# Performance work log

Measured on AMD Instinct MI355X. Metric: run time of the kernel, lower is better.

The kernel has to match this reference:

```python
import jax, jax.numpy as jnp
import numpy as np

B, T, D = 4096, 200, 64
H = 32  # hidden units of score MLP
NEG_INF = jnp.float32(-2**32 + 1)


def setup_inputs() -> dict:
    key = jax.random.key(0)
    k1, k2, k3, k4, k5 = jax.random.split(key, 5)
    query = jax.random.normal(k1, (B, 1, D), dtype=jnp.float32)
    keys = jax.random.normal(k2, (B, T, D), dtype=jnp.float32)
    mask = jax.random.randint(k3, (B, T), 0, 2) > 0
    mask = mask.at[:, 0].set(True)  # ensure at least one valid key per row
    # Glorot-normal-ish init for the tiny score MLP
    W1 = jax.random.normal(k4, (3 * D, H), dtype=jnp.float32) * jnp.sqrt(2.0 / (3 * D + H))
    b1 = jnp.zeros((H,), dtype=jnp.float32)
    W2 = jax.random.normal(k5, (H, 1), dtype=jnp.float32) * jnp.sqrt(2.0 / (H + 1))
    b2 = jnp.zeros((1,), dtype=jnp.float32)
    return {"query": query, "keys": keys, "mask": mask,
            "W1": W1, "b1": b1, "W2": W2, "b2": b2}


def reference(query, keys, mask, W1, b1, W2, b2):
    b, t, d = keys.shape
    q = jnp.broadcast_to(query, (b, t, d))            # tile query over seq
    att_in = jnp.concatenate([q, keys, q - keys], axis=-1)   # [B,T,3D]
    h = jax.nn.sigmoid(att_in @ W1 + b1)              # [B,T,H]
    score = (h @ W2 + b2)[..., 0]                     # [B,T]
    score = jnp.where(mask, score, NEG_INF)
    w = jax.nn.softmax(score, axis=-1)                # [B,T]
    out = jnp.einsum('bt,btd->bd', w, keys)           # weighted key sum
    return out[:, None, :]                            # [B,1,D]
```

## Files before the change

kernel.cpp:

```cpp
#include <hip/hip_runtime.h>
#include <hip/hip_bf16.h>


#define B 4096
#define T 200
#define D 64
#define H 32
#define LOG2E 1.44269504088896340736f
#define SOFF 16.0f

typedef __attribute__((ext_vector_type(8))) short short8;
typedef __attribute__((ext_vector_type(4))) float f32x4;


__global__ __launch_bounds__(256) void prep_kernel(
        const float* __restrict__ W1,
        const float* __restrict__ b1,
        const float* __restrict__ query,
        float*       __restrict__ qa_ws,
        unsigned short* __restrict__ wkf)
{
    int blk = blockIdx.x;
    int n = blk * 256 + threadIdx.x;
    if (blk < (B * H) / 256) {
        int b = n >> 5;
        int j = n & 31;
        const float* qb = query + (size_t)b * D;
        float acc = b1[j];
        #pragma unroll 8
        for (int i = 0; i < D; ++i)
            acc = fmaf(qb[i], W1[i * H + j] + W1[(128 + i) * H + j], acc);
        qa_ws[n] = acc;
    } else {
        int m = n - (B * H);
        int e  = m & 7;
        int l  = (m >> 3) & 63;
        int fs = m >> 9;
        int ntile = fs >> 1, kstep = fs & 1;
        int k = kstep * 32 + (l >> 4) * 8 + e;
        int j = ntile * 16 + (l & 15);
        float v = W1[(64 + k) * H + j] - W1[(128 + k) * H + j];
        __hip_bfloat16 hv = __float2bfloat16(v);
        wkf[m] = __builtin_bit_cast(unsigned short, hv);
    }
}

__device__ __forceinline__ unsigned short bf16u(float x) {
    __hip_bfloat16 h = __float2bfloat16(x);
    return __builtin_bit_cast(unsigned short, h);
}

__global__ __launch_bounds__(256, 5) void attn_pool_kernel(
        const float* __restrict__ keys,
        const int*   __restrict__ mask,
        const unsigned short* __restrict__ wkf,
        const float* __restrict__ qa_all,
        const float* __restrict__ W2,
        float*       __restrict__ out)
{
    __shared__ float part[4][64];
    __shared__ float denw[4];

    const int tid  = threadIdx.x;
    const int b    = blockIdx.x;
    const int wv   = tid >> 6;
    const int lane = tid & 63;
    const int quad = lane >> 4;
    const int l15  = lane & 15;

    const short8* wf = reinterpret_cast<const short8*>(wkf);
    short8 bf0 = wf[0 * 64 + lane];
    short8 bf1 = wf[1 * 64 + lane];
    short8 bf2 = wf[2 * 64 + lane];
    short8 bf3 = wf[3 * 64 + lane];

    const float* qa = qa_all + (size_t)b * H;
    const float qa0 = qa[l15];
    const float qa1 = qa[16 + l15];
    const float w20 = W2[l15];
    const float w21 = W2[16 + l15];

    const float4* krow = reinterpret_cast<const float4*>(keys + (size_t)b * (T * D));
    const int*    mrow = mask + (size_t)b * T;

    float acc[16];
    #pragma unroll
    for (int e = 0; e < 16; ++e) acc[e] = 0.0f;
    float den = 0.0f;

    for (int m0 = wv; m0 < 13; m0 += 4) {
        const int t  = m0 * 16 + l15;
        const int tr = (t < T) ? t : (T - 1);

        float4 k0 = krow[tr * 16 + quad * 2 + 0];
        float4 k1 = krow[tr * 16 + quad * 2 + 1];
        float4 k2 = krow[tr * 16 + 8 + quad * 2 + 0];
        float4 k3 = krow[tr * 16 + 8 + quad * 2 + 1];
        int mval = mrow[tr];

        short8 a0, a1;
        a0[0] = (short)bf16u(k0.x); a0[1] = (short)bf16u(k0.y);
        a0[2] = (short)bf16u(k0.z); a0[3] = (short)bf16u(k0.w);
        a0[4] = (short)bf16u(k1.x); a0[5] = (short)bf16u(k1.y);
        a0[6] = (short)bf16u(k1.z); a0[7] = (short)bf16u(k1.w);
        a1[0] = (short)bf16u(k2.x); a1[1] = (short)bf16u(k2.y);
        a1[2] = (short)bf16u(k2.z); a1[3] = (short)bf16u(k2.w);
        a1[4] = (short)bf16u(k3.x); a1[5] = (short)bf16u(k3.y);
        a1[6] = (short)bf16u(k3.z); a1[7] = (short)bf16u(k3.w);

        f32x4 c0 = {0.f, 0.f, 0.f, 0.f};
        f32x4 c1 = {0.f, 0.f, 0.f, 0.f};
        c0 = __builtin_amdgcn_mfma_f32_16x16x32_bf16(a0, bf0, c0, 0, 0, 0);
        c0 = __builtin_amdgcn_mfma_f32_16x16x32_bf16(a1, bf1, c0, 0, 0, 0);
        c1 = __builtin_amdgcn_mfma_f32_16x16x32_bf16(a0, bf2, c1, 0, 0, 0);
        c1 = __builtin_amdgcn_mfma_f32_16x16x32_bf16(a1, bf3, c1, 0, 0, 0);

        float p[4];
        #pragma unroll
        for (int r = 0; r < 4; ++r) {
            float x0 = c0[r] + qa0;
            float x1 = c1[r] + qa1;
            float s0 = __builtin_amdgcn_rcpf(1.0f + exp2f(-x0 * LOG2E));
            float s1 = __builtin_amdgcn_rcpf(1.0f + exp2f(-x1 * LOG2E));
            p[r] = fmaf(s0, w20, s1 * w21);
        }
        #pragma unroll
        for (int r = 0; r < 4; ++r) {
            #pragma unroll
            for (int off = 1; off <= 8; off <<= 1)
                p[r] += __shfl_xor(p[r], off, 64);
        }
        const int addr = (l15 >> 2) << 6;
        int q0 = __builtin_amdgcn_ds_bpermute(addr, __builtin_bit_cast(int, p[0]));
        int q1 = __builtin_amdgcn_ds_bpermute(addr, __builtin_bit_cast(int, p[1]));
        int q2 = __builtin_amdgcn_ds_bpermute(addr, __builtin_bit_cast(int, p[2]));
        int q3 = __builtin_amdgcn_ds_bpermute(addr, __builtin_bit_cast(int, p[3]));
        const int rsel = l15 & 3;
        int s01 = (rsel & 1) ? q1 : q0;
        int s23 = (rsel & 1) ? q3 : q2;
        float st = __builtin_bit_cast(float, (rsel & 2) ? s23 : s01);

        float w = ((t < T) && (mval != 0)) ? exp2f((st - SOFF) * LOG2E) : 0.0f;
        den += w;

        acc[0]  = fmaf(w, k0.x, acc[0]);  acc[1]  = fmaf(w, k0.y, acc[1]);
        acc[2]  = fmaf(w, k0.z, acc[2]);  acc[3]  = fmaf(w, k0.w, acc[3]);
        acc[4]  = fmaf(w, k1.x, acc[4]);  acc[5]  = fmaf(w, k1.y, acc[5]);
        acc[6]  = fmaf(w, k1.z, acc[6]);  acc[7]  = fmaf(w, k1.w, acc[7]);
        acc[8]  = fmaf(w, k2.x, acc[8]);  acc[9]  = fmaf(w, k2.y, acc[9]);
        acc[10] = fmaf(w, k2.z, acc[10]); acc[11] = fmaf(w, k2.w, acc[11]);
        acc[12] = fmaf(w, k3.x, acc[12]); acc[13] = fmaf(w, k3.y, acc[13]);
        acc[14] = fmaf(w, k3.z, acc[14]); acc[15] = fmaf(w, k3.w, acc[15]);
    }

    #pragma unroll
    for (int off = 1; off <= 8; off <<= 1) {
        #pragma unroll
        for (int e = 0; e < 16; ++e)
            acc[e] += __shfl_xor(acc[e], off, 64);
        den += __shfl_xor(den, off, 64);
    }

    if (l15 == 0) {
        #pragma unroll
        for (int e = 0; e < 8; ++e) {
            part[wv][quad * 8 + e]      = acc[e];
            part[wv][32 + quad * 8 + e] = acc[8 + e];
        }
        if (quad == 0) denw[wv] = den;
    }
    __syncthreads();

    if (tid < 64) {
        float dtot = (denw[0] + denw[1]) + (denw[2] + denw[3]);
        float v = (part[0][tid] + part[1][tid]) + (part[2][tid] + part[3][tid]);
        out[(size_t)b * D + tid] = v * __builtin_amdgcn_rcpf(dtot);
    }
}

extern "C" void kernel_launch(void* const* d_in, const int* in_sizes, int n_in,
                              void* d_out, int out_size, void* d_ws, size_t ws_size,
                              hipStream_t stream) {
    const float* query = (const float*)d_in[0];
    const float* keys  = (const float*)d_in[1];
    const int*   mask  = (const int*)d_in[2];
    const float* W1    = (const float*)d_in[3];
    const float* b1    = (const float*)d_in[4];
    const float* W2    = (const float*)d_in[5];

    float* qa = (float*)d_ws;
    unsigned short* wkf = (unsigned short*)(qa + B * H);

    prep_kernel<<<(B * H) / 256 + 8, 256, 0, stream>>>(W1, b1, query, qa, wkf);
    attn_pool_kernel<<<B, 256, 0, stream>>>(keys, mask, wkf, qa, W2, (float*)d_out);
}
```

Before: 305.1 us.

## Split each batch row into per-wave tiles with atomic accumulation and a finalize pass

Instead of one block per batch row where four waves loop over 13 tiles unevenly, each wave now handles exactly one 16-key tile of one row. Partial numerators are reduced in shared memory and added with global float atomics, and a new finalize kernel divides by the accumulated denominator. The prep kernel also zeroes the accumulation buffers. This is meant to fix load imbalance (13 tiles across 4 waves) and raise parallelism, at the cost of one extra kernel launch, atomic traffic, and nondeterministic summation order.

```diff
diff --git a/kernel.cpp b/kernel.cpp
--- a/kernel.cpp
+++ b/kernel.cpp
@@ -8,6 +8,8 @@
 #define H 32
 #define LOG2E 1.44269504088896340736f
 #define SOFF 16.0f
+#define NTILE 13
+#define PITCH 68
 
 typedef __attribute__((ext_vector_type(8))) short short8;
 typedef __attribute__((ext_vector_type(4))) float f32x4;
@@ -17,12 +19,12 @@
         const float* __restrict__ W1,
         const float* __restrict__ b1,
         const float* __restrict__ query,
-        float*       __restrict__ qa_ws,
-        unsigned short* __restrict__ wkf)
+        float*       __restrict__ ws)
 {
     int blk = blockIdx.x;
-    int n = blk * 256 + threadIdx.x;
-    if (blk < (B * H) / 256) {
+    int tid = threadIdx.x;
+    if (blk < 512) {
+        int n = blk * 256 + tid;
         int b = n >> 5;
         int j = n & 31;
         const float* qb = query + (size_t)b * D;
@@ -30,9 +32,9 @@
         #pragma unroll 8
         for (int i = 0; i < D; ++i)
             acc = fmaf(qb[i], W1[i * H + j] + W1[(128 + i) * H + j], acc);
-        qa_ws[n] = acc;
-    } else {
-        int m = n - (B * H);
+        ws[n] = acc;
+    } else if (blk < 520) {
+        int m = (blk - 512) * 256 + tid;
         int e  = m & 7;
         int l  = (m >> 3) & 63;
         int fs = m >> 9;
@@ -41,7 +43,12 @@
         int j = ntile * 16 + (l & 15);
         float v = W1[(64 + k) * H + j] - W1[(128 + k) * H + j];
         __hip_bfloat16 hv = __float2bfloat16(v);
-        wkf[m] = __builtin_bit_cast(unsigned short, hv);
+        reinterpret_cast<unsigned short*>(ws + 131072)[m] =
+            __builtin_bit_cast(unsigned short, hv);
+    } else {
+        int z = (blk - 520) * 256 + tid;
+        float4 zz = {0.f, 0.f, 0.f, 0.f};
+        reinterpret_cast<float4*>(ws + 132096)[z] = zz;
     }
 }
 
@@ -50,23 +57,26 @@
     return __builtin_bit_cast(unsigned short, h);
 }
 
-__global__ __launch_bounds__(256, 5) void attn_pool_kernel(
+__global__ __launch_bounds__(256) void attn_pool_kernel(
         const float* __restrict__ keys,
         const int*   __restrict__ mask,
         const unsigned short* __restrict__ wkf,
         const float* __restrict__ qa_all,
         const float* __restrict__ W2,
-        float*       __restrict__ out)
+        float*       __restrict__ num,
+        float*       __restrict__ den)
 {
-    __shared__ float part[4][64];
-    __shared__ float denw[4];
+    __shared__ float wkbuf[4][16 * PITCH];
 
     const int tid  = threadIdx.x;
-    const int b    = blockIdx.x;
     const int wv   = tid >> 6;
     const int lane = tid & 63;
     const int quad = lane >> 4;
     const int l15  = lane & 15;
+
+    const int gid  = blockIdx.x * 4 + wv;
+    const int b    = (int)(((unsigned)gid * 20165u) >> 18);
+    const int tile = gid - b * NTILE;
 
     const short8* wf = reinterpret_cast<const short8*>(wkf);
     short8 bf0 = wf[0 * 64 + lane];
@@ -80,102 +90,90 @@
     const float w20 = W2[l15];
     const float w21 = W2[16 + l15];
 
+    const int t  = tile * 16 + l15;
+    const int tr = (t < T) ? t : (T - 1);
+
     const float4* krow = reinterpret_cast<const float4*>(keys + (size_t)b * (T * D));
-    const int*    mrow = mask + (size_t)b * T;
+    float4 k0 = krow[tr * 16 + quad * 2 + 0];
+    float4 k1 = krow[tr * 16 + quad * 2 + 1];
+    float4 k2 = krow[tr * 16 + 8 + quad * 2 + 0];
+    float4 k3 = krow[tr * 16 + 8 + quad * 2 + 1];
+    const int mval = mask[(size_t)b * T + tr];
 
-    float acc[16];
+    short8 a0, a1;
+    a0[0] = (short)bf16u(k0.x); a0[1] = (short)bf16u(k0.y);
+    a0[2] = (short)bf16u(k0.z); a0[3] = (short)bf16u(k0.w);
+    a0[4] = (short)bf16u(k1.x); a0[5] = (short)bf16u(k1.y);
+    a0[6] = (short)bf16u(k1.z); a0[7] = (short)bf16u(k1.w);
+    a1[0] = (short)bf16u(k2.x); a1[1] = (short)bf16u(k2.y);
+    a1[2] = (short)bf16u(k2.z); a1[3] = (short)bf16u(k2.w);
+    a1[4] = (short)bf16u(k3.x); a1[5] = (short)bf16u(k3.y);
+    a1[6] = (short)bf16u(k3.z); a1[7] = (short)bf16u(k3.w);
+
+    f32x4 c0 = {0.f, 0.f, 0.f, 0.f};
+    f32x4 c1 = {0.f, 0.f, 0.f, 0.f};
+    c0 = __builtin_amdgcn_mfma_f32_16x16x32_bf16(a0, bf0, c0, 0, 0, 0);
+    c0 = __builtin_amdgcn_mfma_f32_16x16x32_bf16(a1, bf1, c0, 0, 0, 0);
+    c1 = __builtin_amdgcn_mfma_f32_16x16x32_bf16(a0, bf2, c1, 0, 0, 0);
+    c1 = __builtin_amdgcn_mfma_f32_16x16x32_bf16(a1, bf3, c1, 0, 0, 0);
+
+    float p[4];
     #pragma unroll
-    for (int e = 0; e < 16; ++e) acc[e] = 0.0f;
-    float den = 0.0f;
+    for (int r = 0; r < 4; ++r) {
+        float x0 = c0[r] + qa0;
+        float x1 = c1[r] + qa1;
+        float s0 = __builtin_amdgcn_rcpf(1.0f + exp2f(-x0 * LOG2E));
+        float s1 = __builtin_amdgcn_rcpf(1.0f + exp2f(-x1 * LOG2E));
+        p[r] = fmaf(s0, w20, s1 * w21);
+    }
+    #pragma unroll
+    for (int r = 0; r < 4; ++r) {
+        #pragma unroll
+        for (int off = 1; off <= 8; off <<= 1)
+            p[r] += __shfl_xor(p[r], off, 64);
+    }
+    const int addr = (l15 >> 2) << 6;
+    int q0 = __builtin_amdgcn_ds_bpermute(addr, __builtin_bit_cast(int, p[0]));
+    int q1 = __builtin_amdgcn_ds_bpermute(addr, __builtin_bit_cast(int, p[1]));
+    int q2 = __builtin_amdgcn_ds_bpermute(addr, __builtin_bit_cast(int, p[2]));
+    int q3 = __builtin_amdgcn_ds_bpermute(addr, __builtin_bit_cast(int, p[3]));
+    const int rsel = l15 & 3;
+    int s01 = (rsel & 1) ? q1 : q0;
+    int s23 = (rsel & 1) ? q3 : q2;
+    float st = __builtin_bit_cast(float, (rsel & 2) ? s23 : s01);
 
-    for (int m0 = wv; m0 < 13; m0 += 4) {
-        const int t  = m0 * 16 + l15;
-        const int tr = (t < T) ? t : (T - 1);
+    const float w = ((t < T) && (mval != 0)) ? exp2f((st - SOFF) * LOG2E) : 0.0f;
 
-        float4 k0 = krow[tr * 16 + quad * 2 + 0];
-        float4 k1 = krow[tr * 16 + quad * 2 + 1];
-        float4 k2 = krow[tr * 16 + 8 + quad * 2 + 0];
-        float4 k3 = krow[tr * 16 + 8 + quad * 2 + 1];
-        int mval = mrow[tr];
+    float* wb = wkbuf[wv];
+    float4 wk0 = {w * k0.x, w * k0.y, w * k0.z, w * k0.w};
+    float4 wk1 = {w * k1.x, w * k1.y, w * k1.z, w * k1.w};
+    float4 wk2 = {w * k2.x, w * k2.y, w * k2.z, w * k2.w};
+    float4 wk3 = {w * k3.x, w * k3.y, w * k3.z, w * k3.w};
+    *reinterpret_cast<float4*>(&wb[l15 * PITCH + quad * 8 + 0]) = wk0;
+    *reinterpret_cast<float4*>(&wb[l15 * PITCH + quad * 8 + 4]) = wk1;
+    *reinterpret_cast<float4*>(&wb[l15 * PITCH + 32 + quad * 8 + 0]) = wk2;
+    *reinterpret_cast<float4*>(&wb[l15 * PITCH + 32 + quad * 8 + 4]) = wk3;
 
-        short8 a0, a1;
-        a0[0] = (short)bf16u(k0.x); a0[1] = (short)bf16u(k0.y);
-        a0[2] = (short)bf16u(k0.z); a0[3] = (short)bf16u(k0.w);
-        a0[4] = (short)bf16u(k1.x); a0[5] = (short)bf16u(k1.y);
-        a0[6] = (short)bf16u(k1.z); a0[7] = (short)bf16u(k1.w);
-        a1[0] = (short)bf16u(k2.x); a1[1] = (short)bf16u(k2.y);
-        a1[2] = (short)bf16u(k2.z); a1[3] = (short)bf16u(k2.w);
-        a1[4] = (short)bf16u(k3.x); a1[5] = (short)bf16u(k3.y);
-        a1[6] = (short)bf16u(k3.z); a1[7] = (short)bf16u(k3.w);
+    float dw = w;
+    #pragma unroll
+    for (int off = 1; off <= 8; off <<= 1)
+        dw += __shfl_xor(dw, off, 64);
 
-        f32x4 c0 = {0.f, 0.f, 0.f, 0.f};
-        f32x4 c1 = {0.f, 0.f, 0.f, 0.f};
-        c0 = __builtin_amdgcn_mfma_f32_16x16x32_bf16(a0, bf0, c0, 0, 0, 0);
-        c0 = __builtin_amdgcn_mfma_f32_16x16x32_bf16(a1, bf1, c0, 0, 0, 0);
-        c1 = __builtin_amdgcn_mfma_f32_16x16x32_bf16(a0, bf2, c1, 0, 0, 0);
-        c1 = __builtin_amdgcn_mfma_f32_16x16x32_bf16(a1, bf3, c1, 0, 0, 0);
+    float colsum = 0.0f;
+    #pragma unroll
+    for (int tt = 0; tt < 16; ++tt)
+        colsum += wb[tt * PITCH + lane];
 
-        float p[4];
-        #pragma unroll
-        for (int r = 0; r < 4; ++r) {
-            float x0 = c0[r] + qa0;
-            float x1 = c1[r] + qa1;
-            float s0 = __builtin_amdgcn_rcpf(1.0f + exp2f(-x0 * LOG2E));
-            float s1 = __builtin_amdgcn_rcpf(1.0f + exp2f(-x1 * LOG2E));
-            p[r] = fmaf(s0, w20, s1 * w21);
-        }
-        #pragma unroll
-        for (int r = 0; r < 4; ++r) {
-            #pragma unroll
-            for (int off = 1; off <= 8; off <<= 1)
-                p[r] += __shfl_xor(p[r], off, 64);
-        }
-        const int addr = (l15 >> 2) << 6;
-        int q0 = __builtin_amdgcn_ds_bpermute(addr, __builtin_bit_cast(int, p[0]));
-        int q1 = __builtin_amdgcn_ds_bpermute(addr, __builtin_bit_cast(int, p[1]));
-        int q2 = __builtin_amdgcn_ds_bpermute(addr, __builtin_bit_cast(int, p[2]));
-        int q3 = __builtin_amdgcn_ds_bpermute(addr, __builtin_bit_cast(int, p[3]));
-        const int rsel = l15 & 3;
-        int s01 = (rsel & 1) ? q1 : q0;
-        int s23 = (rsel & 1) ? q3 : q2;
-        float st = __builtin_bit_cast(float, (rsel & 2) ? s23 : s01);
+    atomicAdd(&num[(size_t)b * D + lane], colsum);
+    if (lane == 0) atomicAdd(&den[b], dw);
+}
 
-        float w = ((t < T) && (mval != 0)) ? exp2f((st - SOFF) * LOG2E) : 0.0f;
-        den += w;
-
-        acc[0]  = fmaf(w, k0.x, acc[0]);  acc[1]  = fmaf(w, k0.y, acc[1]);
-        acc[2]  = fmaf(w, k0.z, acc[2]);  acc[3]  = fmaf(w, k0.w, acc[3]);
-        acc[4]  = fmaf(w, k1.x, acc[4]);  acc[5]  = fmaf(w, k1.y, acc[5]);
-        acc[6]  = fmaf(w, k1.z, acc[6]);  acc[7]  = fmaf(w, k1.w, acc[7]);
-        acc[8]  = fmaf(w, k2.x, acc[8]);  acc[9]  = fmaf(w, k2.y, acc[9]);
-        acc[10] = fmaf(w, k2.z, acc[10]); acc[11] = fmaf(w, k2.w, acc[11]);
-        acc[12] = fmaf(w, k3.x, acc[12]); acc[13] = fmaf(w, k3.y, acc[13]);
-        acc[14] = fmaf(w, k3.z, acc[14]); acc[15] = fmaf(w, k3.w, acc[15]);
-    }
-
-    #pragma unroll
-    for (int off = 1; off <= 8; off <<= 1) {
-        #pragma unroll
-        for (int e = 0; e < 16; ++e)
-            acc[e] += __shfl_xor(acc[e], off, 64);
-        den += __shfl_xor(den, off, 64);
-    }
-
-    if (l15 == 0) {
-        #pragma unroll
-        for (int e = 0; e < 8; ++e) {
-            part[wv][quad * 8 + e]      = acc[e];
-            part[wv][32 + quad * 8 + e] = acc[8 + e];
-        }
-        if (quad == 0) denw[wv] = den;
-    }
-    __syncthreads();
-
-    if (tid < 64) {
-        float dtot = (denw[0] + denw[1]) + (denw[2] + denw[3]);
-        float v = (part[0][tid] + part[1][tid]) + (part[2][tid] + part[3][tid]);
-        out[(size_t)b * D + tid] = v * __builtin_amdgcn_rcpf(dtot);
-    }
+__global__ __launch_bounds__(256) void finalize_kernel(
+        const float* __restrict__ num, const float* __restrict__ den,
+        float* __restrict__ out)
+{
+    int i = blockIdx.x * 256 + threadIdx.x;
+    out[i] = num[i] * __builtin_amdgcn_rcpf(den[i >> 6]);
 }
 
 extern "C" void kernel_launch(void* const* d_in, const int* in_sizes, int n_in,
@@ -188,9 +186,14 @@
     const float* b1    = (const float*)d_in[4];
     const float* W2    = (const float*)d_in[5];
 
-    float* qa = (float*)d_ws;
-    unsigned short* wkf = (unsigned short*)(qa + B * H);
+    float* ws = (float*)d_ws;
+    float* qa = ws;
+    unsigned short* wkf = (unsigned short*)(ws + 131072);
+    float* num = ws + 132096;
+    float* den = ws + 132096 + 262144;
 
-    prep_kernel<<<(B * H) / 256 + 8, 256, 0, stream>>>(W1, b1, query, qa, wkf);
-    attn_pool_kernel<<<B, 256, 0, stream>>>(keys, mask, wkf, qa, W2, (float*)d_out);
+    prep_kernel<<<780, 256, 0, stream>>>(W1, b1, query, ws);
+    attn_pool_kernel<<<(B * NTILE) / 4, 256, 0, stream>>>(keys, mask, wkf, qa, W2,
+                                                          num, den);
+    finalize_kernel<<<(B * D) / 256, 256, 0, stream>>>(num, den, (float*)d_out);
 }
```

Measured after the change: 304.0 us. About the same (-0.4%).
